# Kernel tuning notes

Hardware: AMD Instinct MI355X
Metric: run time of the kernel (lower is better)

Reference implementation:

```python
import jax, jax.numpy as jnp
import numpy as np

N_TAGS = 16
START_IX = 14
STOP_IX = 15
NEG = -10000.0

VOCAB = 100000
EMBED = 256
HID = 512          # bidirectional LSTM: per-direction hidden = HID // 2
H = HID // 2
T = 8192


def setup_inputs() -> dict:
    key = jax.random.key(0)
    ks = jax.random.split(key, 16)
    sentence = jax.random.randint(ks[0], (T,), 0, VOCAB)
    embed = jax.random.normal(ks[1], (VOCAB, EMBED), dtype=jnp.float32)
    # PyTorch LSTM params, gate order [i, f, g, o]
    s_ih = 1.0 / np.sqrt(H)
    w_ih_f = jax.random.uniform(ks[2], (4 * H, EMBED), minval=-s_ih, maxval=s_ih)
    w_hh_f = jax.random.uniform(ks[3], (4 * H, H), minval=-s_ih, maxval=s_ih)
    b_ih_f = jax.random.uniform(ks[4], (4 * H,), minval=-s_ih, maxval=s_ih)
    b_hh_f = jax.random.uniform(ks[5], (4 * H,), minval=-s_ih, maxval=s_ih)
    w_ih_b = jax.random.uniform(ks[6], (4 * H, EMBED), minval=-s_ih, maxval=s_ih)
    w_hh_b = jax.random.uniform(ks[7], (4 * H, H), minval=-s_ih, maxval=s_ih)
    b_ih_b = jax.random.uniform(ks[8], (4 * H,), minval=-s_ih, maxval=s_ih)
    b_hh_b = jax.random.uniform(ks[9], (4 * H,), minval=-s_ih, maxval=s_ih)
    # hid2tag linear
    s_o = 1.0 / np.sqrt(HID)
    W_out = jax.random.uniform(ks[10], (N_TAGS, HID), minval=-s_o, maxval=s_o)
    b_out = jax.random.uniform(ks[11], (N_TAGS,), minval=-s_o, maxval=s_o)
    # CRF transition: transition[i, j] = score of j -> i
    transition = jax.random.normal(ks[12], (N_TAGS, N_TAGS), dtype=jnp.float32)
    transition = transition.at[START_IX, :].set(NEG)
    transition = transition.at[:, STOP_IX].set(NEG)
    # random initial hidden state, as in _init_hidden (torch.randn)
    h0 = jax.random.normal(ks[13], (2, H), dtype=jnp.float32)
    c0 = jax.random.normal(ks[14], (2, H), dtype=jnp.float32)
    return {"sentence": sentence, "embed": embed,
            "w_ih_f": w_ih_f, "w_hh_f": w_hh_f, "b_ih_f": b_ih_f, "b_hh_f": b_hh_f,
            "w_ih_b": w_ih_b, "w_hh_b": w_hh_b, "b_ih_b": b_ih_b, "b_hh_b": b_hh_b,
            "W_out": W_out, "b_out": b_out, "transition": transition,
            "h0": h0, "c0": c0}


def _lstm_dir(xw, w_hh, h0, c0):
    # xw: [T, 4H] precomputed input projection (+ both biases)
    def step(carry, xw_t):
        h, c = carry
        z = xw_t + h @ w_hh.T
        i, f, g, o = jnp.split(z, 4)
        i = jax.nn.sigmoid(i)
        f = jax.nn.sigmoid(f)
        g = jnp.tanh(g)
        o = jax.nn.sigmoid(o)
        c = f * c + i * g
        h = o * jnp.tanh(c)
        return (h, c), h
    _, hs = jax.lax.scan(step, (h0, c0), xw)
    return hs  # [T, H]


def _feats(sentence, embed, w_ih_f, w_hh_f, b_ih_f, b_hh_f,
           w_ih_b, w_hh_b, b_ih_b, b_hh_b, W_out, b_out, h0, c0):
    emb = embed[sentence]                                   # [T, E]
    xw_f = emb @ w_ih_f.T + (b_ih_f + b_hh_f)               # [T, 4H]
    hs_f = _lstm_dir(xw_f, w_hh_f, h0[0], c0[0])            # [T, H]
    xw_b = emb[::-1] @ w_ih_b.T + (b_ih_b + b_hh_b)
    hs_b = _lstm_dir(xw_b, w_hh_b, h0[1], c0[1])[::-1]      # [T, H]
    hs = jnp.concatenate([hs_f, hs_b], axis=-1)             # [T, 2H]
    return hs @ W_out.T + b_out                             # [T, n_tags]


def reference(sentence, embed, w_ih_f, w_hh_f, b_ih_f, b_hh_f,
              w_ih_b, w_hh_b, b_ih_b, b_hh_b, W_out, b_out,
              transition, h0, c0):
    feats = _feats(sentence, embed, w_ih_f, w_hh_f, b_ih_f, b_hh_f,
                   w_ih_b, w_hh_b, b_ih_b, b_hh_b, W_out, b_out, h0, c0)

    fv0 = jnp.full((N_TAGS,), NEG, dtype=feats.dtype).at[START_IX].set(0.0)

    def viterbi_step(fv, feat):
        # temp[i, j] = fv[j] + feat[i] + transition[i, j]
        temp = fv[None, :] + feat[:, None] + transition
        return temp.max(axis=1), jnp.argmax(temp, axis=1)

    fv, bps = jax.lax.scan(viterbi_step, fv0, feats)        # bps: [T, n_tags]
    fv = fv + transition[:, STOP_IX]
    id_last = jnp.argmax(fv)

    def backtrack(idc, bp_t):
        return bp_t[idc], idc

    _, path = jax.lax.scan(backtrack, id_last, bps, reverse=True)
    return path  # [T] best tag per timestep
```

## Files before the change

### kernel.cpp

```cpp
#include <hip/hip_runtime.h>
#include <cstdint>
#include <cstddef>

#define T_LEN 8192
#define EMB 256
#define HD 256
#define G4 1024
#define NT 16
#define START_IX 14
#define STOP_IX 15

#define SLICE 8
#define ROWSD 32
#define WPAD 260
#define SENT 0xFFFFFFFFu

struct ScanS {
    float wf[ROWSD * WPAD];
    float wb[ROWSD * WPAD];
    float hf[256];
    float hb[256];
    float part[ROWSD * 17];
    float xwr[16][2][32];
};
struct GemmS {
    float at[32][65];
    float bt[128][65];
};
#define SMEM_BYTES 83968

__device__ __forceinline__ unsigned poll_h(const unsigned* __restrict__ p) {
    unsigned v; int spin = 0;
    do {
        v = __hip_atomic_load(p, __ATOMIC_RELAXED, __HIP_MEMORY_SCOPE_AGENT);
    } while (v == SENT && ++spin < (1 << 20));
    return v;
}

__device__ __forceinline__ unsigned poll_sent(const unsigned* p) {
    unsigned v; int spin = 0;
    do {
        v = __hip_atomic_load(p, __ATOMIC_RELAXED, __HIP_MEMORY_SCOPE_AGENT);
    } while (v == SENT && ++spin < (1 << 20));
    return v;
}

__global__ __launch_bounds__(512) void k_fused(
    const int* __restrict__ sent, const float* __restrict__ embed,
    const float* __restrict__ wih_f, const float* __restrict__ wih_b,
    const float* __restrict__ bih_f, const float* __restrict__ bhh_f,
    const float* __restrict__ bih_b, const float* __restrict__ bhh_b,
    const float* __restrict__ whh_f, const float* __restrict__ whh_b,
    const float* __restrict__ h0, const float* __restrict__ c0,
    float* __restrict__ xw, float* __restrict__ h_hist)
{
    __shared__ __align__(16) char smraw[SMEM_BYTES];
    const int tid = threadIdx.x;

    if ((blockIdx.x & 7) != 0) {
        GemmS* G = (GemmS*)smraw;
        const int f = (blockIdx.x >> 3) * 7 + (blockIdx.x & 7) - 1;
        const int tx = tid & 31, ty = tid >> 5;
        for (int u = f; u < 4096; u += 224) {
            const int t_tile = u >> 4, sub = u & 15;
            const int dir = sub >> 3, r_tile = sub & 7;
            const float* __restrict__ wih = dir ? wih_b : wih_f;
            const float* __restrict__ bih = dir ? bih_b : bih_f;
            const float* __restrict__ bhh = dir ? bhh_b : bhh_f;
            const int t0 = t_tile * 32, r0 = r_tile * 128;
            float acc[2][4] = {};
            for (int k0 = 0; k0 < EMB; k0 += 64) {
                __syncthreads();
                for (int i = tid; i < 32 * 64; i += 512) {
                    int row = i >> 6, k = i & 63;
                    int t = t0 + row;
                    int ts = dir ? (T_LEN - 1 - t) : t;
                    G->at[row][k] = embed[(size_t)sent[ts] * EMB + k0 + k];
                }
                for (int i = tid; i < 128 * 64; i += 512) {
                    int row = i >> 6, k = i & 63;
                    G->bt[row][k] = wih[(size_t)(r0 + row) * EMB + k0 + k];
                }
                __syncthreads();
#pragma unroll 16
                for (int kc = 0; kc < 64; ++kc) {
                    float a[2], b[4];
#pragma unroll
                    for (int v = 0; v < 2; ++v) a[v] = G->at[ty * 2 + v][kc];
#pragma unroll
                    for (int v = 0; v < 4; ++v) b[v] = G->bt[tx * 4 + v][kc];
#pragma unroll
                    for (int v = 0; v < 2; ++v)
#pragma unroll
                        for (int w = 0; w < 4; ++w) acc[v][w] += a[v] * b[w];
                }
            }
#pragma unroll
            for (int v = 0; v < 2; ++v) {
                int t = t0 + ty * 2 + v;
#pragma unroll
                for (int w = 0; w < 4; ++w) {
                    int r = r0 + tx * 4 + w;
                    float val = acc[v][w] + bih[r] + bhh[r];
                    __hip_atomic_store(
                        (unsigned*)&xw[((size_t)dir * T_LEN + t) * G4 + r],
                        __float_as_uint(val),
                        __ATOMIC_RELAXED, __HIP_MEMORY_SCOPE_AGENT);
                }
            }
        }
        return;
    }

    ScanS* S = (ScanS*)smraw;
    const int wsl = blockIdx.x >> 3;
    const int wave = tid >> 6, lane = tid & 63;

    for (int i = tid; i < ROWSD * 256; i += 512) {
        int r = i >> 8, k = i & 255;
        int R = ((r >> 3) << 8) + wsl * SLICE + (r & 7);
        S->wf[r * WPAD + k] = whh_f[(size_t)R * HD + k];
        S->wb[r * WPAD + k] = whh_b[(size_t)R * HD + k];
    }
    if (tid < 256) { S->hf[tid] = h0[tid]; S->hb[tid] = h0[256 + tid]; }
    float c_f = 0.f, c_b = 0.f;
    if (wave == 0 && lane < 8) {
        c_f = c0[wsl * SLICE + lane];
        c_b = c0[256 + wsl * SLICE + lane];
    }
    if (tid < 512) {
        int s = tid >> 6, e = tid & 63, d = e >> 5, row = e & 31;
        int R = ((row >> 3) << 8) + wsl * SLICE + (row & 7);
        unsigned v = poll_sent(
            (const unsigned*)&xw[((size_t)d * T_LEN + s) * G4 + R]);
        S->xwr[s][d][row] = __uint_as_float(v);
    }
    __syncthreads();

    float* __restrict__ hhf = h_hist;
    float* __restrict__ hhb = h_hist + (size_t)T_LEN * HD;

    for (int t = 0; t < T_LEN; ++t) {
        {
            const int q = tid >> 5, rr = tid & 31;
            const float4* wr = (const float4*)&S->wf[rr * WPAD + q * 16];
            const float4* hp = (const float4*)&S->hf[q * 16];
            float a0 = 0.f, a1 = 0.f, a2 = 0.f, a3 = 0.f;
#pragma unroll
            for (int i = 0; i < 4; ++i) {
                float4 wv = wr[i], hv = hp[i];
                a0 += wv.x * hv.x; a1 += wv.y * hv.y;
                a2 += wv.z * hv.z; a3 += wv.w * hv.w;
            }
            S->part[rr * 17 + q] = (a0 + a1) + (a2 + a3);
        }
        __syncthreads();

        if (wave == 0) {
            const int r = lane & 31;
            float xwv = S->xwr[t & 15][0][r];
            if (__builtin_amdgcn_ballot_w64(__float_as_uint(xwv) == SENT)) {
                int R = ((r >> 3) << 8) + wsl * SLICE + (r & 7);
                xwv = __uint_as_float(poll_sent(
                    (const unsigned*)&xw[(size_t)t * G4 + R]));
            }
            float z = xwv;
#pragma unroll
            for (int q = 0; q < 16; ++q) z += S->part[r * 17 + q];
            float a = ((r >> 3) == 2) ? tanhf(z) : 1.f / (1.f + expf(-z));
            const int j = r & 7;
            float af = __shfl(a, 8 + j);
            float ag = __shfl(a, 16 + j);
            float ao = __shfl(a, 24 + j);
            if (lane < 8) {
                c_f = af * c_f + a * ag;
                float hv = ao * tanhf(c_f);
                S->hf[wsl * SLICE + j] = hv;
                __hip_atomic_store(
                    (unsigned*)&hhf[(size_t)t * HD + wsl * SLICE + j],
                    __float_as_uint(hv),
                    __ATOMIC_RELAXED, __HIP_MEMORY_SCOPE_AGENT);
            }
        } else if (wave <= 4) {
            if (t > 0) {
                const int idx = (wave - 1) * 64 + lane;
                if ((idx >> 3) != wsl) {
                    unsigned v = poll_h(
                        (const unsigned*)&hhb[(size_t)(t - 1) * HD + idx]);
                    S->hb[idx] = __uint_as_float(v);
                }
            }
        } else if (wave <= 6) {
            if ((t & 7) == 0 && t + 8 < T_LEN) {
                const int base = (wave - 5) * 64 + lane;
#pragma unroll
                for (int u = 0; u < 4; ++u) {
                    int item = base + u * 128;
                    int s = item >> 6, e = item & 63;
                    int d = e >> 5, row = e & 31;
                    int step = t + 8 + s;
                    int R = ((row >> 3) << 8) + wsl * SLICE + (row & 7);
                    S->xwr[step & 15][d][row] =
                        xw[((size_t)d * T_LEN + step) * G4 + R];
                }
            }
        }
        __syncthreads();

        {
            const int q = tid >> 5, rr = tid & 31;
            const float4* wr = (const float4*)&S->wb[rr * WPAD + q * 16];
            const float4* hp = (const float4*)&S->hb[q * 16];
            float a0 = 0.f, a1 = 0.f, a2 = 0.f, a3 = 0.f;
#pragma unroll
            for (int i = 0; i < 4; ++i) {
                float4 wv = wr[i], hv = hp[i];
                a0 += wv.x * hv.x; a1 += wv.y * hv.y;
                a2 += wv.z * hv.z; a3 += wv.w * hv.w;
            }
            S->part[rr * 17 + q] = (a0 + a1) + (a2 + a3);
        }
        __syncthreads();

        if (wave == 0) {
            const int r = lane & 31;
            float xwv = S->xwr[t & 15][1][r];
            if (__builtin_amdgcn_ballot_w64(__float_as_uint(xwv) == SENT)) {
                int R = ((r >> 3) << 8) + wsl * SLICE + (r & 7);
                xwv = __uint_as_float(poll_sent((const unsigned*)
                    &xw[((size_t)T_LEN + t) * G4 + R]));
            }
            float z = xwv;
#pragma unroll
            for (int q = 0; q < 16; ++q) z += S->part[r * 17 + q];
            float a = ((r >> 3) == 2) ? tanhf(z) : 1.f / (1.f + expf(-z));
            const int j = r & 7;
            float af = __shfl(a, 8 + j);
            float ag = __shfl(a, 16 + j);
            float ao = __shfl(a, 24 + j);
            if (lane < 8) {
                c_b = af * c_b + a * ag;
                float hv = ao * tanhf(c_b);
                S->hb[wsl * SLICE + j] = hv;
                __hip_atomic_store(
                    (unsigned*)&hhb[(size_t)t * HD + wsl * SLICE + j],
                    __float_as_uint(hv),
                    __ATOMIC_RELAXED, __HIP_MEMORY_SCOPE_AGENT);
            }
        } else if (wave <= 4) {
            const int idx = (wave - 1) * 64 + lane;
            if ((idx >> 3) != wsl) {
                unsigned v = poll_h(
                    (const unsigned*)&hhf[(size_t)t * HD + idx]);
                S->hf[idx] = __uint_as_float(v);
            }
        }
        __syncthreads();
    }
}

__global__ __launch_bounds__(256) void k_feats(
    const float* __restrict__ h_hist, const float* __restrict__ Wout,
    const float* __restrict__ bout, float* __restrict__ feats)
{
    __shared__ float wlds[16][512];
    const int tid = threadIdx.x;
    for (int i = tid; i < 16 * 512; i += 256) wlds[i >> 9][i & 511] = Wout[i];
    __syncthreads();
    const int idx = blockIdx.x * 256 + tid;
    const int t = idx >> 4, tg = idx & 15;
    const float4* hf = (const float4*)(h_hist + (size_t)t * HD);
    const float4* hb = (const float4*)(h_hist + (size_t)(T_LEN + (T_LEN - 1 - t)) * HD);
    float acc = bout[tg];
    for (int k = 0; k < 64; ++k) {
        float4 a = hf[k];
        float4 b = *(const float4*)&wlds[tg][k * 4];
        acc += a.x * b.x + a.y * b.y + a.z * b.z + a.w * b.w;
    }
    for (int k = 0; k < 64; ++k) {
        float4 a = hb[k];
        float4 b = *(const float4*)&wlds[tg][256 + k * 4];
        acc += a.x * b.x + a.y * b.y + a.z * b.z + a.w * b.w;
    }
    feats[(size_t)t * NT + tg] = acc;
}

template <int CTRL>
__device__ __forceinline__ float dpp_qf(float x) {
    return __int_as_float(__builtin_amdgcn_update_dpp(
        0, __float_as_int(x), CTRL, 0xF, 0xF, true));
}
template <int CTRL>
__device__ __forceinline__ int dpp_qi(int x) {
    return __builtin_amdgcn_update_dpp(0, x, CTRL, 0xF, 0xF, true);
}
#define QP_SWAP1 0xB1
#define QP_SWAP2 0x4E

__device__ __forceinline__ unsigned bsel16(uint4 g, unsigned e) {
    unsigned wd = (e < 8u) ? ((e < 4u) ? g.x : g.y) : ((e < 12u) ? g.z : g.w);
    return (wd >> ((e & 3u) * 8u)) & 15u;
}

__global__ __launch_bounds__(256) void k_viterbi(
    const float* __restrict__ feats, const float* __restrict__ trans,
    int* __restrict__ out, unsigned char* __restrict__ bp)
{
    __shared__ int sid;
    __shared__ unsigned slo[512], shi[512];
    __shared__ float fbuf[2][256][16];
    const int tid = threadIdx.x;
    const int wave = tid >> 6, lane = tid & 63;
    const int i = lane >> 2, jq = lane & 3;

    for (int idx = tid; idx < 4096; idx += 256)
        fbuf[0][idx >> 4][idx & 15] = feats[idx];

    float tr[4];
    if (wave == 0) {
#pragma unroll
        for (int u = 0; u < 4; ++u) tr[u] = trans[i * 16 + jq * 4 + u];
    }
    float fvn = (i == START_IX) ? 0.0f : -10000.0f;
    __syncthreads();

    for (int chunk = 0; chunk < T_LEN / 256; ++chunk) {
        const int b = chunk & 1;
        const int base = chunk * 256;
        if (wave == 0) {
            float fA = fbuf[b][0][i];
            float fB = fbuf[b][1][i];
            for (int s = 0; s < 256; ++s) {
                float fC = (s + 2 < 256) ? fbuf[b][s + 2][i] : 0.f;

                float best = -3.4e38f; int bj = 0;
#pragma unroll
                for (int u = 0; u < 4; ++u) {
                    float fvj = __shfl(fvn, (jq * 4 + u) * 4);
                    float v = (fvj + fA) + tr[u];
                    if (v > best) { best = v; bj = jq * 4 + u; }
                }
                {
                    float ob = dpp_qf<QP_SWAP1>(best);
                    int   oj = dpp_qi<QP_SWAP1>(bj);
                    if (ob > best || (ob == best && oj < bj)) { best = ob; bj = oj; }
                    ob = dpp_qf<QP_SWAP2>(best);
                    oj = dpp_qi<QP_SWAP2>(bj);
                    if (ob > best || (ob == best && oj < bj)) { best = ob; bj = oj; }
                }
                if (jq == 0) bp[(size_t)(base + s) * 16 + i] = (unsigned char)bj;
                fvn = best;
                fA = fB; fB = fC;
            }
        } else if (chunk + 1 < T_LEN / 256) {
            const int nb = b ^ 1;
            const size_t noff = (size_t)(base + 256) * 16;
            for (int idx = (wave - 1) * 64 + lane; idx < 4096; idx += 192)
                fbuf[nb][idx >> 4][idx & 15] = feats[noff + idx];
        }
        __syncthreads();
    }

    if (wave == 0) {
        float fvi = __shfl(fvn, (lane & 15) * 4);
        float term = (lane < 16) ? fvi + trans[lane * 16 + STOP_IX] : -3.4e38f;
        int ti = lane;
#pragma unroll
        for (int off = 1; off < 16; off <<= 1) {
            float ov = __shfl_xor(term, off); int oi = __shfl_xor(ti, off);
            if (ov > term || (ov == term && oi < ti)) { term = ov; ti = oi; }
        }
        if (lane == 0) sid = ti;
    }
    __syncthreads();

    const int j = tid;
    unsigned Flo = 0x76543210u, Fhi = 0xfedcba98u;
    for (int t = 32 * j + 31; t >= 32 * j; --t) {
        uint4 g = *(const uint4*)&bp[(size_t)t * 16];
        unsigned nlo = 0, nhi = 0;
#pragma unroll
        for (int x = 0; x < 8; ++x) {
            unsigned e = (Flo >> (x * 4)) & 15u;
            nlo |= bsel16(g, e) << (x * 4);
        }
#pragma unroll
        for (int x = 0; x < 8; ++x) {
            unsigned e = (Fhi >> (x * 4)) & 15u;
            nhi |= bsel16(g, e) << (x * 4);
        }
        Flo = nlo; Fhi = nhi;
    }
    slo[j] = Flo; shi[j] = Fhi;
    slo[j + 256] = 0x76543210u; shi[j + 256] = 0xfedcba98u;
    __syncthreads();
    for (int off = 1; off < 256; off <<= 1) {
        unsigned alo = slo[j], ahi = shi[j];
        unsigned blo = slo[j + off], bhi = shi[j + off];
        __syncthreads();
        unsigned nlo = 0, nhi = 0;
#pragma unroll
        for (int x = 0; x < 8; ++x) {
            unsigned e = (blo >> (x * 4)) & 15u;
            unsigned rr = ((e < 8u ? alo : ahi) >> ((e & 7u) * 4u)) & 15u;
            nlo |= rr << (x * 4);
        }
#pragma unroll
        for (int x = 0; x < 8; ++x) {
            unsigned e = (bhi >> (x * 4)) & 15u;
            unsigned rr = ((e < 8u ? alo : ahi) >> ((e & 7u) * 4u)) & 15u;
            nhi |= rr << (x * 4);
        }
        slo[j] = nlo; shi[j] = nhi;
        __syncthreads();
    }
    int idl = sid;
    unsigned plo = slo[j + 1], phi = shi[j + 1];
    unsigned x = (((unsigned)idl < 8u ? plo : phi) >> (((unsigned)idl & 7u) * 4u)) & 15u;
    out[32 * j + 31] = (int)x;
    for (int t = 32 * j + 30; t >= 32 * j; --t) {
        x = (unsigned)bp[(size_t)(t + 1) * 16 + x];
        out[t] = (int)x;
    }
}

extern "C" void kernel_launch(void* const* d_in, const int* in_sizes, int n_in,
                              void* d_out, int out_size, void* d_ws, size_t ws_size,
                              hipStream_t stream) {
    const int*   sent  = (const int*)  d_in[0];
    const float* embed = (const float*)d_in[1];
    const float* wih_f = (const float*)d_in[2];
    const float* whh_f = (const float*)d_in[3];
    const float* bih_f = (const float*)d_in[4];
    const float* bhh_f = (const float*)d_in[5];
    const float* wih_b = (const float*)d_in[6];
    const float* whh_b = (const float*)d_in[7];
    const float* bih_b = (const float*)d_in[8];
    const float* bhh_b = (const float*)d_in[9];
    const float* Wout  = (const float*)d_in[10];
    const float* bout  = (const float*)d_in[11];
    const float* trans = (const float*)d_in[12];
    const float* h0    = (const float*)d_in[13];
    const float* c0    = (const float*)d_in[14];
    int* out = (int*)d_out;

    float* ws_xw   = (float*)d_ws;
    float* ws_h    = ws_xw + (size_t)2 * T_LEN * G4;
    float* ws_feat = ws_h + (size_t)2 * T_LEN * HD;
    unsigned char* ws_bp = (unsigned char*)(ws_feat + (size_t)T_LEN * NT);

    hipMemsetAsync(ws_xw, 0xFF, (size_t)2 * T_LEN * G4 * sizeof(float), stream);
    hipMemsetAsync(ws_h, 0xFF, (size_t)2 * T_LEN * HD * sizeof(float), stream);

    k_fused<<<256, 512, 0, stream>>>(sent, embed, wih_f, wih_b,
                                     bih_f, bhh_f, bih_b, bhh_b,
                                     whh_f, whh_b, h0, c0,
                                     ws_xw, ws_h);
    k_feats<<<512, 256, 0, stream>>>(ws_h, Wout, bout, ws_feat);
    k_viterbi<<<1, 256, 0, stream>>>(ws_feat, trans, out, ws_bp);
}
```

Measured before the change: 12.84 ms.

## Merge forward and backward LSTM step phases into one synchronized phase

Folds the forward and backward recurrent matvecs into a single pass over a combined 64-row weight tile, with each wave covering a 32-wide k-slice for both directions. The two gate updates now run in parallel on waves 0 and 1, and both directions' h exchanges are polled together in one phase. This cuts the per-timestep barriers from four to three and overlaps the cross-block waits of the two directions. The cost is longer per-thread dot products and a different layout for the partial sums.

```diff
diff --git a/kernel.cpp b/kernel.cpp
--- a/kernel.cpp
+++ b/kernel.cpp
@@ -11,16 +11,15 @@
 #define STOP_IX 15
 
 #define SLICE 8
-#define ROWSD 32
+#define ROWS2 64
 #define WPAD 260
 #define SENT 0xFFFFFFFFu
 
 struct ScanS {
-    float wf[ROWSD * WPAD];
-    float wb[ROWSD * WPAD];
+    float w[ROWS2 * WPAD];
     float hf[256];
     float hb[256];
-    float part[ROWSD * 17];
+    float part[ROWS2 * 9];
     float xwr[16][2][32];
 };
 struct GemmS {
@@ -116,18 +115,16 @@
     const int wsl = blockIdx.x >> 3;
     const int wave = tid >> 6, lane = tid & 63;
 
-    for (int i = tid; i < ROWSD * 256; i += 512) {
+    for (int i = tid; i < ROWS2 * 256; i += 512) {
         int r = i >> 8, k = i & 255;
-        int R = ((r >> 3) << 8) + wsl * SLICE + (r & 7);
-        S->wf[r * WPAD + k] = whh_f[(size_t)R * HD + k];
-        S->wb[r * WPAD + k] = whh_b[(size_t)R * HD + k];
+        int d = r >> 5, lr = r & 31;
+        int R = ((lr >> 3) << 8) + wsl * SLICE + (lr & 7);
+        S->w[r * WPAD + k] = (d ? whh_b : whh_f)[(size_t)R * HD + k];
     }
     if (tid < 256) { S->hf[tid] = h0[tid]; S->hb[tid] = h0[256 + tid]; }
     float c_f = 0.f, c_b = 0.f;
-    if (wave == 0 && lane < 8) {
-        c_f = c0[wsl * SLICE + lane];
-        c_b = c0[256 + wsl * SLICE + lane];
-    }
+    if (wave == 0 && lane < 8) c_f = c0[wsl * SLICE + lane];
+    if (wave == 1 && lane < 8) c_b = c0[256 + wsl * SLICE + lane];
     if (tid < 512) {
         int s = tid >> 6, e = tid & 63, d = e >> 5, row = e & 31;
         int R = ((row >> 3) << 8) + wsl * SLICE + (row & 7);
@@ -142,17 +139,17 @@
 
     for (int t = 0; t < T_LEN; ++t) {
         {
-            const int q = tid >> 5, rr = tid & 31;
-            const float4* wr = (const float4*)&S->wf[rr * WPAD + q * 16];
-            const float4* hp = (const float4*)&S->hf[q * 16];
+            const float4* wr = (const float4*)&S->w[lane * WPAD + wave * 32];
+            const float4* hp = (const float4*)
+                ((lane < 32 ? S->hf : S->hb) + wave * 32);
             float a0 = 0.f, a1 = 0.f, a2 = 0.f, a3 = 0.f;
 #pragma unroll
-            for (int i = 0; i < 4; ++i) {
+            for (int i = 0; i < 8; ++i) {
                 float4 wv = wr[i], hv = hp[i];
                 a0 += wv.x * hv.x; a1 += wv.y * hv.y;
                 a2 += wv.z * hv.z; a3 += wv.w * hv.w;
             }
-            S->part[rr * 17 + q] = (a0 + a1) + (a2 + a3);
+            S->part[lane * 9 + wave] = (a0 + a1) + (a2 + a3);
         }
         __syncthreads();
 
@@ -166,7 +163,7 @@
             }
             float z = xwv;
 #pragma unroll
-            for (int q = 0; q < 16; ++q) z += S->part[r * 17 + q];
+            for (int s = 0; s < 8; ++s) z += S->part[r * 9 + s];
             float a = ((r >> 3) == 2) ? tanhf(z) : 1.f / (1.f + expf(-z));
             const int j = r & 7;
             float af = __shfl(a, 8 + j);
@@ -181,48 +178,7 @@
                     __float_as_uint(hv),
                     __ATOMIC_RELAXED, __HIP_MEMORY_SCOPE_AGENT);
             }
-        } else if (wave <= 4) {
-            if (t > 0) {
-                const int idx = (wave - 1) * 64 + lane;
-                if ((idx >> 3) != wsl) {
-                    unsigned v = poll_h(
-                        (const unsigned*)&hhb[(size_t)(t - 1) * HD + idx]);
-                    S->hb[idx] = __uint_as_float(v);
-                }
-            }
-        } else if (wave <= 6) {
-            if ((t & 7) == 0 && t + 8 < T_LEN) {
-                const int base = (wave - 5) * 64 + lane;
-#pragma unroll
-                for (int u = 0; u < 4; ++u) {
-                    int item = base + u * 128;
-                    int s = item >> 6, e = item & 63;
-                    int d = e >> 5, row = e & 31;
-                    int step = t + 8 + s;
-                    int R = ((row >> 3) << 8) + wsl * SLICE + (row & 7);
-                    S->xwr[step & 15][d][row] =
-                        xw[((size_t)d * T_LEN + step) * G4 + R];
-                }
-            }
-        }
-        __syncthreads();
-
-        {
-            const int q = tid >> 5, rr = tid & 31;
-            const float4* wr = (const float4*)&S->wb[rr * WPAD + q * 16];
-            const float4* hp = (const float4*)&S->hb[q * 16];
-            float a0 = 0.f, a1 = 0.f, a2 = 0.f, a3 = 0.f;
-#pragma unroll
-            for (int i = 0; i < 4; ++i) {
-                float4 wv = wr[i], hv = hp[i];
-                a0 += wv.x * hv.x; a1 += wv.y * hv.y;
-                a2 += wv.z * hv.z; a3 += wv.w * hv.w;
-            }
-            S->part[rr * 17 + q] = (a0 + a1) + (a2 + a3);
-        }
-        __syncthreads();
-
-        if (wave == 0) {
+        } else if (wave == 1) {
             const int r = lane & 31;
             float xwv = S->xwr[t & 15][1][r];
             if (__builtin_amdgcn_ballot_w64(__float_as_uint(xwv) == SENT)) {
@@ -232,7 +188,7 @@
             }
             float z = xwv;
 #pragma unroll
-            for (int q = 0; q < 16; ++q) z += S->part[r * 17 + q];
+            for (int s = 0; s < 8; ++s) z += S->part[(32 + r) * 9 + s];
             float a = ((r >> 3) == 2) ? tanhf(z) : 1.f / (1.f + expf(-z));
             const int j = r & 7;
             float af = __shfl(a, 8 + j);
@@ -247,12 +203,37 @@
                     __float_as_uint(hv),
                     __ATOMIC_RELAXED, __HIP_MEMORY_SCOPE_AGENT);
             }
-        } else if (wave <= 4) {
-            const int idx = (wave - 1) * 64 + lane;
-            if ((idx >> 3) != wsl) {
-                unsigned v = poll_h(
-                    (const unsigned*)&hhf[(size_t)t * HD + idx]);
-                S->hf[idx] = __uint_as_float(v);
+        } else if (wave == 5 || wave == 6) {
+            if ((t & 7) == 0 && t + 8 < T_LEN) {
+                const int base = (wave - 5) * 64 + lane;
+#pragma unroll
+                for (int u = 0; u < 4; ++u) {
+                    int item = base + u * 128;
+                    int s = item >> 6, e = item & 63;
+                    int d = e >> 5, row = e & 31;
+                    int step = t + 8 + s;
+                    int R = ((row >> 3) << 8) + wsl * SLICE + (row & 7);
+                    S->xwr[step & 15][d][row] =
+                        xw[((size_t)d * T_LEN + step) * G4 + R];
+                }
+            }
+        }
+        __syncthreads();
+
+        if (t + 1 < T_LEN) {
+            if (tid < 256) {
+                if ((tid >> 3) != wsl) {
+                    unsigned v = poll_h(
+                        (const unsigned*)&hhf[(size_t)t * HD + tid]);
+                    S->hf[tid] = __uint_as_float(v);
+                }
+            } else {
+                const int e = tid - 256;
+                if ((e >> 3) != wsl) {
+                    unsigned v = poll_h(
+                        (const unsigned*)&hhb[(size_t)t * HD + e]);
+                    S->hb[e] = __uint_as_float(v);
+                }
             }
         }
         __syncthreads();
```

New measurement: 17.11 ms. 1.33x slower.
